# Kernel tuning notes

Measured on AMD Instinct MI355X. Metric: run time of the kernel, lower is better.

## Reference

```python
import jax, jax.numpy as jnp
import numpy as np

B = 32768      # batch
D = 2          # input_dim
H = 2048       # hidden_dim
NQ = 4         # qubits


def setup_inputs() -> dict:
    key = jax.random.key(0)
    ks = jax.random.split(key, 14)

    def lin(k, fan_in, fan_out):
        # kaiming-uniform-ish init like nn.Linear
        bound = 1.0 / np.sqrt(fan_in)
        kw, kb = jax.random.split(k)
        W = jax.random.uniform(kw, (fan_in, fan_out), jnp.float32, -bound, bound)
        b = jax.random.uniform(kb, (fan_out,), jnp.float32, -bound, bound)
        return W, b

    x = jax.random.normal(ks[0], (B, D), jnp.float32)
    W1, b1 = lin(ks[1], D + NQ, H)      # core Linear 1
    W2, b2 = lin(ks[2], H, H)           # core Linear 2
    Wc, bc = lin(ks[3], H, 1)           # classifier
    Wr1, br1 = lin(ks[4], D, 8)
    Wr2, br2 = lin(ks[5], 8, 4)
    Wr3, br3 = lin(ks[6], 4, 1)
    return dict(x=x, W1=W1, b1=b1, W2=W2, b2=b2, Wc=Wc, bc=bc,
                Wr1=Wr1, br1=br1, Wr2=Wr2, br2=br2, Wr3=Wr3, br3=br3)


def _quantum_feature_map(x):
    # Exact closed form of: RY(x_i) on 4 qubits from |0000>, CNOT(0,1), CNOT(2,3),
    # expval(PauliZ(i)). Padding with zeros -> cos(0)=1 on unused wires.
    xq = jnp.pad(x, ((0, 0), (0, NQ - x.shape[1])))  # [B,4]
    c = jnp.cos(xq)
    return jnp.stack([c[:, 0], c[:, 0] * c[:, 1], c[:, 2], c[:, 2] * c[:, 3]], axis=1)


def reference(x, W1, b1, W2, b2, Wc, bc, Wr1, br1, Wr2, br2, Wr3, br3):
    qfeat = _quantum_feature_map(x)               # [B,4]
    concat = jnp.concatenate([x, qfeat], axis=1)  # [B, D+4]
    h = jnp.tanh(concat @ W1 + b1)                # [B,H]
    h = jnp.tanh(h @ W2 + b2)                     # [B,H]
    logits = h @ Wc + bc                          # [B,1]
    r = jnp.tanh(x @ Wr1 + br1)
    r = jnp.tanh(r @ Wr2 + br2)
    risk = r @ Wr3 + br3                          # [B,1]
    return logits, risk
```

## Files before the change

kernel.cpp:

```cpp
#include <hip/hip_runtime.h>
#include <hip/hip_bf16.h>
#include <stdint.h>

#define B_ROWS 32768
#define HID    2048
#define K_DIM  2048

#define BM 128
#define BN 256
#define BKB 128

#define SCALE_W   5747.3639f
#define DEQUANT   1.3700225e-6f

typedef __bf16 bf16x8_t __attribute__((ext_vector_type(8)));
typedef int    int4v    __attribute__((ext_vector_type(4)));
typedef char   char8    __attribute__((ext_vector_type(8)));

__device__ __forceinline__ float fast_tanh(float x) {
    float e = __expf(2.0f * x);
    return 1.0f - 2.0f * __builtin_amdgcn_rcpf(e + 1.0f);
}

__device__ __forceinline__ void gl_lds16(const void* g, void* l) {
    __builtin_amdgcn_global_load_lds(
        (const __attribute__((address_space(1))) void*)(uintptr_t)g,
        (__attribute__((address_space(3))) void*)(uint32_t)(uintptr_t)l,
        16, 0, 0);
}

__global__ __launch_bounds__(256) void transpose_w2_kernel(
    const float* __restrict__ W2, char* __restrict__ W2t) {
    __shared__ float tile[32][33];
    const int n0 = blockIdx.x * 32;
    const int k0 = blockIdx.y * 32;
    const int tx = threadIdx.x;
    const int ty = threadIdx.y;
#pragma unroll
    for (int i = 0; i < 4; ++i) {
        int k = k0 + ty + i * 8;
        tile[ty + i * 8][tx] = W2[(size_t)k * HID + n0 + tx];
    }
    __syncthreads();
#pragma unroll
    for (int i = 0; i < 4; ++i) {
        int n = n0 + ty + i * 8;
        W2t[(size_t)n * K_DIM + k0 + tx] =
            (char)__float2int_rn(tile[tx][ty + i * 8] * SCALE_W);
    }
}

__global__ __launch_bounds__(256) void layer1_kernel(
    const float* __restrict__ x,   const float* __restrict__ W1, const float* __restrict__ b1,
    const float* __restrict__ Wr1, const float* __restrict__ br1,
    const float* __restrict__ Wr2, const float* __restrict__ br2,
    const float* __restrict__ Wr3, const float* __restrict__ br3,
    const float* __restrict__ bc,
    char* __restrict__ h1, float* __restrict__ out) {
    const int t  = threadIdx.x;
    const int n0 = t * 8;
    float w0[8], w1[8], w2[8], w3[8], wb[8];
#pragma unroll
    for (int j = 0; j < 8; ++j) {
        w0[j] = W1[0 * HID + n0 + j];
        w1[j] = W1[1 * HID + n0 + j];
        w2[j] = W1[2 * HID + n0 + j];
        w3[j] = W1[3 * HID + n0 + j];
        wb[j] = W1[4 * HID + n0 + j] + W1[5 * HID + n0 + j] + b1[n0 + j];
    }
    const int brow0 = blockIdx.x * 32;
    for (int r = 0; r < 32; ++r) {
        const int b = brow0 + r;
        const float x0 = x[2 * b], x1 = x[2 * b + 1];
        const float c0 = cosf(x0);
        const float cc = c0 * cosf(x1);
        char8 v;
#pragma unroll
        for (int j = 0; j < 8; ++j) {
            float z = wb[j] + x0 * w0[j] + x1 * w1[j] + c0 * w2[j] + cc * w3[j];
            v[j] = (char)__float2int_rn(fast_tanh(z) * 127.0f);
        }
        *(char8*)(h1 + (size_t)b * HID + n0) = v;
    }
    if (t < 32) {
        const int b = brow0 + t;
        const float x0 = x[2 * b], x1 = x[2 * b + 1];
        float r1[8];
#pragma unroll
        for (int j = 0; j < 8; ++j)
            r1[j] = fast_tanh(br1[j] + x0 * Wr1[j] + x1 * Wr1[8 + j]);
        float r2[4];
#pragma unroll
        for (int j = 0; j < 4; ++j) {
            float s = br2[j];
#pragma unroll
            for (int i = 0; i < 8; ++i) s += r1[i] * Wr2[i * 4 + j];
            r2[j] = fast_tanh(s);
        }
        float risk = br3[0];
#pragma unroll
        for (int i = 0; i < 4; ++i) risk += r2[i] * Wr3[i];
        out[B_ROWS + b] = risk;
        out[b]          = bc[0];
    }
}

__global__ __launch_bounds__(256, 2) void gemm_kernel(
    const char* __restrict__ A,
    const char* __restrict__ Bt,
    const float* __restrict__ b2, const float* __restrict__ Wc,
    float* __restrict__ out) {
    __shared__ __align__(16) char sA[BM * BKB];
    __shared__ __align__(16) char sB[BN * BKB];

    const int tid  = threadIdx.x;
    const int wave = tid >> 6;
    const int lane = tid & 63;
    const int bid  = blockIdx.x;
    const int m0 = (bid >> 3) * BM;
    const int n0 = (bid & 7) * BN;

    const char* aSrc[4]; char* aDst[4];
    const char* bSrc[8]; char* bDst[8];
    {
        const int rsub  = lane >> 3;
        const int chunk = (lane & 7) ^ rsub;
#pragma unroll
        for (int i = 0; i < 4; ++i) {
            int seg = wave * 4 + i;
            aSrc[i] = A + (size_t)(m0 + seg * 8 + rsub) * K_DIM + chunk * 16;
            aDst[i] = sA + seg * 1024;
        }
#pragma unroll
        for (int i = 0; i < 8; ++i) {
            int seg = wave * 8 + i;
            bSrc[i] = Bt + (size_t)(n0 + seg * 8 + rsub) * K_DIM + chunk * 16;
            bDst[i] = sB + seg * 1024;
        }
    }

    int4v acc[4][8] = {};
    const int mw   = (wave & 1) * 64;
    const int nw   = (wave >> 1) * 128;
    const int quad = lane >> 4;
    const int r16  = lane & 15;
    const int x7   = lane & 7;

    for (int kb = 0; kb < K_DIM; kb += BKB) {
#pragma unroll
        for (int i = 0; i < 4; ++i) gl_lds16(aSrc[i] + kb, aDst[i]);
#pragma unroll
        for (int i = 0; i < 8; ++i) gl_lds16(bSrc[i] + kb, bDst[i]);
        __syncthreads();
#pragma unroll
        for (int ks = 0; ks < 2; ++ks) {
            const int slot = ((ks * 4 + quad) ^ x7) * 16;
            int4v af[4], bfr[8];
#pragma unroll
            for (int mi = 0; mi < 4; ++mi)
                af[mi]  = *(const int4v*)(sA + (mw + mi * 16 + r16) * BKB + slot);
#pragma unroll
            for (int ni = 0; ni < 8; ++ni)
                bfr[ni] = *(const int4v*)(sB + (nw + ni * 16 + r16) * BKB + slot);
#pragma unroll
            for (int mi = 0; mi < 4; ++mi)
#pragma unroll
                for (int ni = 0; ni < 8; ++ni)
                    acc[mi][ni] = __builtin_amdgcn_mfma_i32_16x16x64_i8(
                        af[mi], bfr[ni], acc[mi][ni], 0, 0, 0);
        }
        __syncthreads();
    }

    float b2v[8], wcv[8];
#pragma unroll
    for (int ni = 0; ni < 8; ++ni) {
        int gn = n0 + nw + ni * 16 + r16;
        b2v[ni] = b2[gn];
        wcv[ni] = Wc[gn];
    }
#pragma unroll
    for (int mi = 0; mi < 4; ++mi) {
#pragma unroll
        for (int r = 0; r < 4; ++r) {
            int gm = m0 + mw + mi * 16 + quad * 4 + r;
            float rs = 0.f;
#pragma unroll
            for (int ni = 0; ni < 8; ++ni)
                rs += fast_tanh((float)acc[mi][ni][r] * DEQUANT + b2v[ni]) * wcv[ni];
            rs += __shfl_xor(rs, 1);
            rs += __shfl_xor(rs, 2);
            rs += __shfl_xor(rs, 4);
            rs += __shfl_xor(rs, 8);
            if (r16 == 0) atomicAdd(&out[gm], rs);
        }
    }
}

extern "C" void kernel_launch(void* const* d_in, const int* in_sizes, int n_in,
                              void* d_out, int out_size, void* d_ws, size_t ws_size,
                              hipStream_t stream) {
    const float* x   = (const float*)d_in[0];
    const float* W1  = (const float*)d_in[1];
    const float* b1  = (const float*)d_in[2];
    const float* W2  = (const float*)d_in[3];
    const float* b2  = (const float*)d_in[4];
    const float* Wc  = (const float*)d_in[5];
    const float* bc  = (const float*)d_in[6];
    const float* Wr1 = (const float*)d_in[7];
    const float* br1 = (const float*)d_in[8];
    const float* Wr2 = (const float*)d_in[9];
    const float* br2 = (const float*)d_in[10];
    const float* Wr3 = (const float*)d_in[11];
    const float* br3 = (const float*)d_in[12];
    float* out = (float*)d_out;

    char* W2t = (char*)d_ws;
    char* h1  = (char*)d_ws + (size_t)4 * 1024 * 1024;

    transpose_w2_kernel<<<dim3(HID / 32, K_DIM / 32), dim3(32, 8), 0, stream>>>(W2, W2t);
    layer1_kernel<<<B_ROWS / 32, 256, 0, stream>>>(x, W1, b1, Wr1, br1, Wr2, br2,
                                                   Wr3, br3, bc, h1, out);
    gemm_kernel<<<(B_ROWS / BM) * (HID / BN), 256, 0, stream>>>(h1, W2t, b2, Wc, out);
}
```

Measured before the change: 269.0 us.

## Merge transpose and layer1 into one launch; shrink GEMM tile to 128x128 with two waves

Folds the W2 quantize-transpose kernel into the layer1 kernel as extra blocks, so a single launch replaces two. Changes the int8 GEMM from 256-thread 128x256 tiles to 128-thread 128x128 tiles, doubling the block count. Each wave still computes a 64x128 sub-tile, but LDS use per block drops from 48 KB to 32 KB, which should allow more resident blocks. The cost is less operand reuse per block, so more global and L2 traffic for A and B, and twice as many partial-sum atomics to the output.

```diff
diff --git a/kernel.cpp b/kernel.cpp
--- a/kernel.cpp
+++ b/kernel.cpp
@@ -6,16 +6,17 @@
 #define HID    2048
 #define K_DIM  2048
 
-#define BM 128
-#define BN 256
+#define BT  128
 #define BKB 128
 
 #define SCALE_W   5747.3639f
 #define DEQUANT   1.3700225e-6f
 
-typedef __bf16 bf16x8_t __attribute__((ext_vector_type(8)));
-typedef int    int4v    __attribute__((ext_vector_type(4)));
-typedef char   char8    __attribute__((ext_vector_type(8)));
+#define L1_BLOCKS (B_ROWS / 32)
+#define TR_BLOCKS ((HID/32)*(K_DIM/32))
+
+typedef int  int4v __attribute__((ext_vector_type(4)));
+typedef char char8 __attribute__((ext_vector_type(8)));
 
 __device__ __forceinline__ float fast_tanh(float x) {
     float e = __expf(2.0f * x);
@@ -29,35 +30,36 @@
         16, 0, 0);
 }
 
-__global__ __launch_bounds__(256) void transpose_w2_kernel(
-    const float* __restrict__ W2, char* __restrict__ W2t) {
-    __shared__ float tile[32][33];
-    const int n0 = blockIdx.x * 32;
-    const int k0 = blockIdx.y * 32;
-    const int tx = threadIdx.x;
-    const int ty = threadIdx.y;
-#pragma unroll
-    for (int i = 0; i < 4; ++i) {
-        int k = k0 + ty + i * 8;
-        tile[ty + i * 8][tx] = W2[(size_t)k * HID + n0 + tx];
-    }
-    __syncthreads();
-#pragma unroll
-    for (int i = 0; i < 4; ++i) {
-        int n = n0 + ty + i * 8;
-        W2t[(size_t)n * K_DIM + k0 + tx] =
-            (char)__float2int_rn(tile[tx][ty + i * 8] * SCALE_W);
-    }
-}
-
-__global__ __launch_bounds__(256) void layer1_kernel(
+__global__ __launch_bounds__(256) void prep_kernel(
     const float* __restrict__ x,   const float* __restrict__ W1, const float* __restrict__ b1,
+    const float* __restrict__ W2,
     const float* __restrict__ Wr1, const float* __restrict__ br1,
     const float* __restrict__ Wr2, const float* __restrict__ br2,
     const float* __restrict__ Wr3, const float* __restrict__ br3,
     const float* __restrict__ bc,
-    char* __restrict__ h1, float* __restrict__ out) {
-    const int t  = threadIdx.x;
+    char* __restrict__ h1, char* __restrict__ W2t, float* __restrict__ out) {
+    const int t = threadIdx.x;
+    if (blockIdx.x >= L1_BLOCKS) {
+        __shared__ float tile[32][33];
+        const int tb = blockIdx.x - L1_BLOCKS;
+        const int n0 = (tb & 63) * 32;
+        const int k0 = (tb >> 6) * 32;
+        const int tx = t & 31;
+        const int ty = t >> 5;
+#pragma unroll
+        for (int i = 0; i < 4; ++i) {
+            int k = k0 + ty + i * 8;
+            tile[ty + i * 8][tx] = W2[(size_t)k * HID + n0 + tx];
+        }
+        __syncthreads();
+#pragma unroll
+        for (int i = 0; i < 4; ++i) {
+            int n = n0 + ty + i * 8;
+            W2t[(size_t)n * K_DIM + k0 + tx] =
+                (char)__float2int_rn(tile[tx][ty + i * 8] * SCALE_W);
+        }
+        return;
+    }
     const int n0 = t * 8;
     float w0[8], w1[8], w2[8], w3[8], wb[8];
 #pragma unroll
@@ -105,52 +107,48 @@
     }
 }
 
-__global__ __launch_bounds__(256, 2) void gemm_kernel(
+__global__ __launch_bounds__(128, 2) void gemm_kernel(
     const char* __restrict__ A,
     const char* __restrict__ Bt,
     const float* __restrict__ b2, const float* __restrict__ Wc,
     float* __restrict__ out) {
-    __shared__ __align__(16) char sA[BM * BKB];
-    __shared__ __align__(16) char sB[BN * BKB];
+    __shared__ __align__(16) char sA[BT * BKB];
+    __shared__ __align__(16) char sB[BT * BKB];
 
     const int tid  = threadIdx.x;
     const int wave = tid >> 6;
     const int lane = tid & 63;
     const int bid  = blockIdx.x;
-    const int m0 = (bid >> 3) * BM;
-    const int n0 = (bid & 7) * BN;
-
-    const char* aSrc[4]; char* aDst[4];
+    const int m0 = (bid >> 4) * BT;
+    const int n0 = (bid & 15) * BT;
+
+    const char* aSrc[8]; char* aDst[8];
     const char* bSrc[8]; char* bDst[8];
     {
         const int rsub  = lane >> 3;
         const int chunk = (lane & 7) ^ rsub;
 #pragma unroll
-        for (int i = 0; i < 4; ++i) {
-            int seg = wave * 4 + i;
+        for (int i = 0; i < 8; ++i) {
+            int seg = wave * 8 + i;
             aSrc[i] = A + (size_t)(m0 + seg * 8 + rsub) * K_DIM + chunk * 16;
             aDst[i] = sA + seg * 1024;
-        }
-#pragma unroll
-        for (int i = 0; i < 8; ++i) {
-            int seg = wave * 8 + i;
             bSrc[i] = Bt + (size_t)(n0 + seg * 8 + rsub) * K_DIM + chunk * 16;
             bDst[i] = sB + seg * 1024;
         }
     }
 
     int4v acc[4][8] = {};
-    const int mw   = (wave & 1) * 64;
-    const int nw   = (wave >> 1) * 128;
+    const int mw   = wave * 64;
     const int quad = lane >> 4;
     const int r16  = lane & 15;
     const int x7   = lane & 7;
 
-    for (int kb = 0; kb < K_DIM; kb += BKB) {
-#pragma unroll
-        for (int i = 0; i < 4; ++i) gl_lds16(aSrc[i] + kb, aDst[i]);
-#pragma unroll
-        for (int i = 0; i < 8; ++i) gl_lds16(bSrc[i] + kb, bDst[i]);
+    for (int kb = 0; kb < K_DIM / BKB; ++kb) {
+#pragma unroll
+        for (int i = 0; i < 8; ++i) {
+            gl_lds16(aSrc[i], aDst[i]);  aSrc[i] += BKB;
+            gl_lds16(bSrc[i], bDst[i]);  bSrc[i] += BKB;
+        }
         __syncthreads();
 #pragma unroll
         for (int ks = 0; ks < 2; ++ks) {
@@ -161,7 +159,7 @@
                 af[mi]  = *(const int4v*)(sA + (mw + mi * 16 + r16) * BKB + slot);
 #pragma unroll
             for (int ni = 0; ni < 8; ++ni)
-                bfr[ni] = *(const int4v*)(sB + (nw + ni * 16 + r16) * BKB + slot);
+                bfr[ni] = *(const int4v*)(sB + (ni * 16 + r16) * BKB + slot);
 #pragma unroll
             for (int mi = 0; mi < 4; ++mi)
 #pragma unroll
@@ -175,7 +173,7 @@
     float b2v[8], wcv[8];
 #pragma unroll
     for (int ni = 0; ni < 8; ++ni) {
-        int gn = n0 + nw + ni * 16 + r16;
+        int gn = n0 + ni * 16 + r16;
         b2v[ni] = b2[gn];
         wcv[ni] = Wc[gn];
     }
@@ -218,8 +216,7 @@
     char* W2t = (char*)d_ws;
     char* h1  = (char*)d_ws + (size_t)4 * 1024 * 1024;
 
-    transpose_w2_kernel<<<dim3(HID / 32, K_DIM / 32), dim3(32, 8), 0, stream>>>(W2, W2t);
-    layer1_kernel<<<B_ROWS / 32, 256, 0, stream>>>(x, W1, b1, Wr1, br1, Wr2, br2,
-                                                   Wr3, br3, bc, h1, out);
-    gemm_kernel<<<(B_ROWS / BM) * (HID / BN), 256, 0, stream>>>(h1, W2t, b2, Wc, out);
-}
+    prep_kernel<<<L1_BLOCKS + TR_BLOCKS, 256, 0, stream>>>(
+        x, W1, b1, W2, Wr1, br1, Wr2, br2, Wr3, br3, bc, h1, W2t, out);
+    gemm_kernel<<<(B_ROWS / BT) * (HID / BT), 128, 0, stream>>>(h1, W2t, b2, Wc, out);
+}
```

Result: slower. 277.9 us (+3.3%).
